# Kernel optimization log

Hardware: AMD Instinct MI355X
Metric: run time of the kernel (lower is better)

Reference implementation:

```python
import jax, jax.numpy as jnp
import numpy as np


def setup_inputs() -> dict:
    key = jax.random.key(0)
    k1, k2, k3 = jax.random.split(key, 3)
    B, D_IN, HIDDEN = 4096, 1024, 32768  # hidden = d_in * scale_size(32)
    x = jax.random.normal(k1, (B, D_IN), dtype=jnp.float32)
    W_enc = jax.random.normal(k2, (HIDDEN, D_IN), dtype=jnp.float32) * (1.0 / np.sqrt(D_IN))
    b_enc = jnp.zeros((HIDDEN,), dtype=jnp.float32)  # encoder.bias.data.zero_()
    # W_dec = encoder.weight.clone() then unit-norm rows (set_decoder_norm_to_unit_norm)
    W_dec = jax.random.normal(k3, (HIDDEN, D_IN), dtype=jnp.float32)
    W_dec = W_dec / (jnp.linalg.norm(W_dec, axis=1, keepdims=True) + jnp.finfo(jnp.float32).eps)
    b_dec = jnp.zeros((D_IN,), dtype=jnp.float32)
    return {"x": x, "W_enc": W_enc, "b_enc": b_enc, "W_dec": W_dec, "b_dec": b_dec, "k": 32}


def reference(x, W_enc, b_enc, W_dec, b_dec, k):
    # sae_in = x - b_dec; pre_acts = relu(encoder(sae_in))
    sae_in = x - b_dec
    pre_acts = jax.nn.relu(jnp.einsum('bd,hd->bh', sae_in, W_enc) + b_enc)  # [B, H]
    # topk_activation: keep top-k per row, zero elsewhere, then z @ W_dec.
    # Equivalent sparse decode: gather the k rows of W_dec and contract.
    topk_vals, topk_idx = jax.lax.top_k(pre_acts, k)  # [B, k]
    # x_reconstructed = z @ W_dec + b_dec  (z is the dense scatter of topk)
    x_rec = jnp.einsum('bk,bkd->bd', topk_vals, W_dec[topk_idx]) + b_dec
    return x_rec
```

## Files before the change

kernel.cpp:

```cpp
#include <hip/hip_runtime.h>
#include <hip/hip_bf16.h>
#include <stdint.h>
#include <stddef.h>


#define BROWS 4096
#define DIN   1024
#define HID   32768
#define KTOP  32
#define KC    48
#define PT    16

#define BM 256
#define BN 256
#define BK 64
#define NT (DIN / BK)

typedef short short8_t __attribute__((ext_vector_type(8)));
typedef float fx4 __attribute__((ext_vector_type(4)));

__device__ __forceinline__ unsigned short f2bf(float f) {
  unsigned u = __float_as_uint(f);
  u += 0x7FFFu + ((u >> 16) & 1u);
  return (unsigned short)(u >> 16);
}

__global__ __launch_bounds__(256) void conv_wc(const float* __restrict__ W,
                                               unsigned short* __restrict__ Wbc, int c0) {
  int base = (blockIdx.x * 256 + threadIdx.x) * 4;
  float4 v = *(const float4*)(W + (size_t)c0 * DIN + base);
  ushort4 o;
  o.x = f2bf(v.x); o.y = f2bf(v.y); o.z = f2bf(v.z); o.w = f2bf(v.w);
  *(ushort4*)(Wbc + base) = o;
}

__global__ __launch_bounds__(256) void prep_x(const float* __restrict__ x,
                                              const float* __restrict__ bdec,
                                              unsigned short* __restrict__ xbf) {
  int base = (blockIdx.x * 256 + threadIdx.x) * 4;
  int col = base & (DIN - 1);
  float4 xv = *(const float4*)(x + base);
  float4 bv = *(const float4*)(bdec + col);
  ushort4 o;
  o.x = f2bf(xv.x - bv.x); o.y = f2bf(xv.y - bv.y);
  o.z = f2bf(xv.z - bv.z); o.w = f2bf(xv.w - bv.w);
  *(ushort4*)(xbf + base) = o;
}

__global__ __launch_bounds__(256) void init_cand(unsigned* __restrict__ cand) {
  int i = blockIdx.x * 256 + threadIdx.x;
  if (i < BROWS * KC) cand[i] = 0u;
}


__device__ __forceinline__ void stage_half(const unsigned short* __restrict__ g0,
                                           unsigned short* l0, int t, int k0) {
  const int w6 = (t >> 6) << 6;
#pragma unroll
  for (int i = 0; i < 2; ++i) {
    const int l  = i * 512 + t;
    const int r  = l >> 3;
    const int cl = (l & 7) ^ (r & 7);
    const unsigned short* g = g0 + (size_t)r * DIN + k0 + cl * 8;
    unsigned short* ld = l0 + (size_t)(i * 512 + w6) * 8;
    __builtin_amdgcn_global_load_lds((const __attribute__((address_space(1))) unsigned int*)g,
                                     (__attribute__((address_space(3))) unsigned int*)ld,
                                     16, 0, 0);
  }
}

__device__ __forceinline__ void tile_step(int tt,
                                          const unsigned short* __restrict__ Ab,
                                          const unsigned short* __restrict__ Wb,
                                          unsigned short* bc, unsigned short* bn,
                                          fx4 (&acc)[8][4],
                                          int t, int l16, int quad, int wm, int wn) {
  const int k1 = (tt + 1) * BK;
  const int k2 = (tt + 2) * BK;
  if (tt < NT - 1) { asm volatile("s_waitcnt vmcnt(4)" ::: "memory"); }
  else             { asm volatile("s_waitcnt vmcnt(0)" ::: "memory"); }
  __builtin_amdgcn_s_barrier();
  const unsigned short* Ar = bc + wm * 8192;
  const unsigned short* Br = bc + 16384;
  short8_t a0[8], a1[8], bfv[4][2];
#pragma unroll
  for (int mt = 0; mt < 8; ++mt)
    a0[mt] = *(const short8_t*)(Ar + (mt * 16 + l16) * 64 + ((quad) ^ (l16 & 7)) * 8);
#pragma unroll
  for (int nt = 0; nt < 4; ++nt)
#pragma unroll
    for (int ks = 0; ks < 2; ++ks)
      bfv[nt][ks] = *(const short8_t*)(Br + (wn * 64 + nt * 16 + l16) * 64 +
                                       ((ks * 4 + quad) ^ (l16 & 7)) * 8);
  if (tt + 1 < NT) stage_half(Wb, bn + 16384, t, k1);
  __builtin_amdgcn_s_setprio(1);
#pragma unroll
  for (int mt = 0; mt < 8; ++mt) {
    acc[mt][0] = __builtin_amdgcn_mfma_f32_16x16x32_bf16(a0[mt], bfv[0][0], acc[mt][0], 0, 0, 0);
    acc[mt][1] = __builtin_amdgcn_mfma_f32_16x16x32_bf16(a0[mt], bfv[1][0], acc[mt][1], 0, 0, 0);
  }
  __builtin_amdgcn_s_setprio(0);
  __builtin_amdgcn_s_barrier();
  if (tt + 1 < NT) stage_half(Wb + 128 * DIN, bn + 24576, t, k1);
  __builtin_amdgcn_s_setprio(1);
#pragma unroll
  for (int mt = 0; mt < 8; ++mt) {
    acc[mt][2] = __builtin_amdgcn_mfma_f32_16x16x32_bf16(a0[mt], bfv[2][0], acc[mt][2], 0, 0, 0);
    acc[mt][3] = __builtin_amdgcn_mfma_f32_16x16x32_bf16(a0[mt], bfv[3][0], acc[mt][3], 0, 0, 0);
  }
  __builtin_amdgcn_s_setprio(0);
  __builtin_amdgcn_s_barrier();
#pragma unroll
  for (int mt = 0; mt < 8; ++mt)
    a1[mt] = *(const short8_t*)(Ar + (mt * 16 + l16) * 64 + ((4 + quad) ^ (l16 & 7)) * 8);
#pragma unroll
  for (int mt = 0; mt < 8; ++mt) { asm volatile("" : "+v"(a1[mt])); }
  __builtin_amdgcn_sched_barrier(0);
  __builtin_amdgcn_s_barrier();
  if (tt + 2 < NT) stage_half(Ab, bc, t, k2);
  __builtin_amdgcn_s_setprio(1);
#pragma unroll
  for (int mt = 0; mt < 8; ++mt) {
    acc[mt][0] = __builtin_amdgcn_mfma_f32_16x16x32_bf16(a1[mt], bfv[0][1], acc[mt][0], 0, 0, 0);
    acc[mt][1] = __builtin_amdgcn_mfma_f32_16x16x32_bf16(a1[mt], bfv[1][1], acc[mt][1], 0, 0, 0);
  }
  __builtin_amdgcn_s_setprio(0);
  __builtin_amdgcn_s_barrier();
  if (tt + 2 < NT) stage_half(Ab + 128 * DIN, bc + 8192, t, k2);
  __builtin_amdgcn_s_setprio(1);
#pragma unroll
  for (int mt = 0; mt < 8; ++mt) {
    acc[mt][2] = __builtin_amdgcn_mfma_f32_16x16x32_bf16(a1[mt], bfv[2][1], acc[mt][2], 0, 0, 0);
    acc[mt][3] = __builtin_amdgcn_mfma_f32_16x16x32_bf16(a1[mt], bfv[3][1], acc[mt][3], 0, 0, 0);
  }
  __builtin_amdgcn_s_setprio(0);
  __builtin_amdgcn_s_barrier();
}

__global__ __launch_bounds__(512, 2) void gemm_scores(
    const unsigned short* __restrict__ A,
    const unsigned short* __restrict__ W,
    const float* __restrict__ benc,
    unsigned short* __restrict__ scores,
    int Hc, int c0) {
  extern __shared__ unsigned short lds[];
  const int t    = threadIdx.x;
  const int lane = t & 63;
  const int wv   = t >> 6;
  const int wm   = wv >> 2;
  const int wn   = wv & 3;
  const int l16  = lane & 15;
  const int quad = lane >> 4;

  const int nwg  = (int)(gridDim.x * gridDim.y);
  const int orig = (int)(blockIdx.y * gridDim.x + blockIdx.x);
  const int q    = nwg >> 3, r8 = nwg & 7;
  const int xcd  = orig & 7, loc = orig >> 3;
  const int swz  = (xcd < r8 ? xcd * (q + 1) : r8 * (q + 1) + (xcd - r8) * q) + loc;
  const int bx   = swz % (int)gridDim.x;
  const int by   = swz / (int)gridDim.x;

  const int row0  = by * BM;
  const int colc0 = bx * BN;
  const unsigned short* Ab = A + (size_t)row0 * DIN;
  const unsigned short* Wb = W + (size_t)colc0 * DIN;

  unsigned short* buf0 = lds;
  unsigned short* buf1 = lds + 32768;

  fx4 acc[8][4];
  fx4 zero = {0.f, 0.f, 0.f, 0.f};
#pragma unroll
  for (int i = 0; i < 8; ++i)
#pragma unroll
    for (int j = 0; j < 4; ++j) acc[i][j] = zero;

  stage_half(Ab,            buf0,         t, 0);
  stage_half(Ab + 128*DIN,  buf0 + 8192,  t, 0);
  stage_half(Wb,            buf0 + 16384, t, 0);
  stage_half(Wb + 128*DIN,  buf0 + 24576, t, 0);
  stage_half(Ab,            buf1,         t, BK);
  stage_half(Ab + 128*DIN,  buf1 + 8192,  t, BK);

#pragma unroll 1
  for (int it = 0; it < NT / 2; ++it) {
    tile_step(2 * it,     Ab, Wb, buf0, buf1, acc, t, l16, quad, wm, wn);
    tile_step(2 * it + 1, Ab, Wb, buf1, buf0, acc, t, l16, quad, wm, wn);
  }

  const int colbase = colc0 + wn * 64;
  float bval[4];
#pragma unroll
  for (int nt = 0; nt < 4; ++nt) bval[nt] = benc[c0 + colbase + nt * 16 + l16];

  unsigned short* et = lds;
#pragma unroll
  for (int c = 0; c < 2; ++c) {
    __syncthreads();
    if (wm == c) {
#pragma unroll
      for (int mt = 0; mt < 8; ++mt)
#pragma unroll
        for (int nt = 0; nt < 4; ++nt) {
          const int col = wn * 64 + nt * 16 + l16;
          const int ch = col >> 3, cw = col & 7;
#pragma unroll
          for (int rg = 0; rg < 4; ++rg) {
            const int row = mt * 16 + quad * 4 + rg;
            float v = acc[mt][nt][rg] + bval[nt];
            et[row * 256 + ((ch ^ quad) * 8) + cw] = f2bf(v > 0.f ? v : 0.f);
          }
        }
    }
    __syncthreads();
    {
      const int row = t >> 2;
      const int cb  = (t & 3) * 8;
      const int xq  = (row >> 2) & 3;
      const size_t gro = (size_t)(row0 + c * 128 + row) * Hc + colc0;
#pragma unroll
      for (int i = 0; i < 8; ++i) {
        const int ch = cb + i;
        short8_t v = *(const short8_t*)(et + row * 256 + ((ch ^ xq) * 8));
        *(short8_t*)(scores + gro + ch * 8) = v;
      }
    }
  }
}

__global__ __launch_bounds__(128) void topk_cand(const unsigned short* __restrict__ scores,
                                                 int Hc, int c0,
                                                 unsigned* __restrict__ cand) {
  __shared__ unsigned lk[128 * 17];
  const int row = blockIdx.x;
  const int t = threadIdx.x;
  unsigned s[PT];
#pragma unroll
  for (int j = 0; j < PT; ++j) s[j] = 0u;

  const unsigned short* srow = scores + (size_t)row * Hc;
  for (int cb = t * 8; cb < Hc; cb += 128 * 8) {
    short8_t v = *(const short8_t*)(srow + cb);
    int gcb = c0 + cb;
#pragma unroll
    for (int e = 0; e < 8; ++e) {
      unsigned val = (unsigned)(unsigned short)v[e];
      unsigned key = (val << 16) | (unsigned)(0x7FFF - (gcb + e));
      if (key > s[PT - 1]) {
        unsigned prev = 0xFFFFFFFFu;
#pragma unroll
        for (int j = 0; j < PT; ++j) {
          unsigned sj = s[j];
          s[j] = (sj >= key) ? sj : (prev < key ? prev : key);
          prev = sj;
        }
      }
    }
  }
  if (t < KC) {
    unsigned key = cand[row * KC + t];
    if (key > s[PT - 1]) {
      unsigned prev = 0xFFFFFFFFu;
#pragma unroll
      for (int j = 0; j < PT; ++j) {
        unsigned sj = s[j];
        s[j] = (sj >= key) ? sj : (prev < key ? prev : key);
        prev = sj;
      }
    }
  }
#pragma unroll
  for (int j = 0; j < PT; ++j) lk[t * 17 + j] = s[j];
  __syncthreads();

  if (t < 64) {
    unsigned k0 = lk[t * 17];
    unsigned k1 = lk[(t + 64) * 17];
    int h0 = 0, h1 = 0;
    unsigned mywin = 0;
    for (int it = 0; it < KC; ++it) {
      unsigned wmax = (k0 > k1) ? k0 : k1;
#pragma unroll
      for (int off = 32; off >= 1; off >>= 1) {
        unsigned o = __shfl_down(wmax, (unsigned)off);
        if (o > wmax) wmax = o;
      }
      wmax = __shfl(wmax, 0);
      if (it == t) mywin = wmax;
      if (k0 == wmax)      { ++h0; k0 = (h0 < PT) ? lk[t * 17 + h0] : 0u; }
      else if (k1 == wmax) { ++h1; k1 = (h1 < PT) ? lk[(t + 64) * 17 + h1] : 0u; }
    }
    if (t < KC) cand[row * KC + t] = mywin;
  }
}

__global__ __launch_bounds__(256) void rescore_decode(
    const unsigned* __restrict__ cand,
    const float* __restrict__ x, const float* __restrict__ Wenc,
    const float* __restrict__ benc,
    const float* __restrict__ Wdec, const float* __restrict__ bdec,
    float* __restrict__ out) {
  __shared__ float xr[DIN];
  __shared__ double sc[KC];
  __shared__ int   scol[KC];
  __shared__ float fv[KTOP];
  __shared__ int   fi[KTOP];
  const int row = blockIdx.x, t = threadIdx.x;

  {
    float4 xv = *(const float4*)(x + (size_t)row * DIN + t * 4);
    float4 bv = *(const float4*)(bdec + t * 4);
    *(float4*)(xr + t * 4) = make_float4(xv.x - bv.x, xv.y - bv.y, xv.z - bv.z, xv.w - bv.w);
  }
  if (t < KC) scol[t] = 0x7FFF - (int)(cand[row * KC + t] & 0xFFFFu);
  if (t < KTOP) { fv[t] = 0.f; fi[t] = 0; }
  __syncthreads();

  const int wave = t >> 6, lane = t & 63;
  for (int j = wave; j < KC; j += 4) {
    int col = scol[j];
    const float* wr = Wenc + (size_t)col * DIN;
    double p = 0.0;
#pragma unroll
    for (int q = 0; q < 4; ++q) {
      int o = q * 256 + lane * 4;
      float4 w = *(const float4*)(wr + o);
      float4 xv = *(const float4*)(xr + o);
      p += (double)xv.x * (double)w.x + (double)xv.y * (double)w.y +
           (double)xv.z * (double)w.z + (double)xv.w * (double)w.w;
    }
#pragma unroll
    for (int off = 32; off >= 1; off >>= 1) p += __shfl_down(p, off);
    if (lane == 0) {
      double v = p + (double)benc[col];
      sc[j] = v > 0.0 ? v : 0.0;
    }
  }
  __syncthreads();

  if (t < KC) {
    double mv = sc[t];
    int mc = scol[t];
    int rank = 0;
    for (int j = 0; j < KC; ++j) {
      double oj = sc[j];
      if (oj > mv || (oj == mv && (scol[j] < mc || (scol[j] == mc && j < t)))) ++rank;
    }
    if (rank < KTOP) { fv[rank] = (float)mv; fi[rank] = mc; }
  }
  __syncthreads();

  const int c = t * 4;
  float4 bd = *(const float4*)(bdec + c);
  float a0 = bd.x, a1 = bd.y, a2 = bd.z, a3 = bd.w;
#pragma unroll 8
  for (int j = 0; j < KTOP; ++j) {
    float v = fv[j];
    float4 w = *(const float4*)(Wdec + (size_t)fi[j] * DIN + c);
    a0 += v * w.x; a1 += v * w.y; a2 += v * w.z; a3 += v * w.w;
  }
  *(float4*)(out + (size_t)row * DIN + c) = make_float4(a0, a1, a2, a3);
}

extern "C" void kernel_launch(void* const* d_in, const int* in_sizes, int n_in,
                              void* d_out, int out_size, void* d_ws, size_t ws_size,
                              hipStream_t stream) {
  const float* x    = (const float*)d_in[0];
  const float* Wenc = (const float*)d_in[1];
  const float* benc = (const float*)d_in[2];
  const float* Wdec = (const float*)d_in[3];
  const float* bdec = (const float*)d_in[4];
  float* out = (float*)d_out;

  char* ws = (char*)d_ws;
  unsigned short* xbf  = (unsigned short*)ws;
  unsigned*       cand = (unsigned*)(ws + (8u << 20));

  const size_t fixed = (size_t)(9u << 20);
  int Hc = HID;
  while (Hc > 256 &&
         fixed + (size_t)Hc * DIN * 2 + (size_t)BROWS * Hc * 2 > ws_size)
    Hc >>= 1;

  unsigned short* Wbc    = (unsigned short*)(ws + fixed);
  unsigned short* scores = (unsigned short*)(ws + fixed + (size_t)Hc * DIN * 2);

  static bool attr_set = false;
  if (!attr_set) {
    (void)hipFuncSetAttribute((const void*)gemm_scores,
                              hipFuncAttributeMaxDynamicSharedMemorySize, 131072);
    attr_set = true;
  }

  prep_x<<<BROWS * DIN / 1024, 256, 0, stream>>>(x, bdec, xbf);
  init_cand<<<(BROWS * KC + 255) / 256, 256, 0, stream>>>(cand);
  for (int c0 = 0; c0 < HID; c0 += Hc) {
    conv_wc<<<Hc, 256, 0, stream>>>(Wenc, Wbc, c0);
    gemm_scores<<<dim3(Hc / BN, BROWS / BM), 512, 131072, stream>>>(xbf, Wbc, benc, scores, Hc, c0);
    topk_cand<<<BROWS, 128, 0, stream>>>(scores, Hc, c0, cand);
  }
  rescore_decode<<<BROWS, 256, 0, stream>>>(cand, x, Wenc, benc, Wdec, bdec, out);
}
```

Measured before the change: 1.119 ms.

## Reload MFMA fragments per phase to cut register pressure, pad epilogue LDS

The GEMM inner step now keeps one set of A fragments and two B fragments at a time, reloading them from LDS before each half of the tile rather than holding a0/a1 plus all eight B fragments. Extra barriers are added so the prefetch of the next A tile can be moved to the final phase and issued as one batch. The epilogue staging buffer changes from an XOR swizzle to a padded row stride. The goal is to lower VGPR pressure and simplify addressing, at the cost of more LDS reads and more barriers per tile step.

Result: faster. 1.020 ms (-8.8%).

```diff
diff --git a/kernel.cpp b/kernel.cpp
--- a/kernel.cpp
+++ b/kernel.cpp
@@ -15,6 +15,7 @@
 #define BN 256
 #define BK 64
 #define NT (DIN / BK)
+#define EP 264
 
 typedef short short8_t __attribute__((ext_vector_type(8)));
 typedef float fx4 __attribute__((ext_vector_type(4)));
@@ -80,59 +81,73 @@
   if (tt < NT - 1) { asm volatile("s_waitcnt vmcnt(4)" ::: "memory"); }
   else             { asm volatile("s_waitcnt vmcnt(0)" ::: "memory"); }
   __builtin_amdgcn_s_barrier();
+
   const unsigned short* Ar = bc + wm * 8192;
-  const unsigned short* Br = bc + 16384;
-  short8_t a0[8], a1[8], bfv[4][2];
-#pragma unroll
-  for (int mt = 0; mt < 8; ++mt)
-    a0[mt] = *(const short8_t*)(Ar + (mt * 16 + l16) * 64 + ((quad) ^ (l16 & 7)) * 8);
-#pragma unroll
-  for (int nt = 0; nt < 4; ++nt)
-#pragma unroll
-    for (int ks = 0; ks < 2; ++ks)
-      bfv[nt][ks] = *(const short8_t*)(Br + (wn * 64 + nt * 16 + l16) * 64 +
-                                       ((ks * 4 + quad) ^ (l16 & 7)) * 8);
+  const unsigned short* Br = bc + 16384 + (wn * 64 + l16) * 64;
+  const int xs = l16 & 7;
+  short8_t a[8], b0, b1;
+
+#pragma unroll
+  for (int mt = 0; mt < 8; ++mt)
+    a[mt] = *(const short8_t*)(Ar + (mt * 16 + l16) * 64 + ((quad ^ xs) * 8));
+  b0 = *(const short8_t*)(Br + 0 * 1024 + ((quad ^ xs) * 8));
+  b1 = *(const short8_t*)(Br + 1 * 1024 + ((quad ^ xs) * 8));
   if (tt + 1 < NT) stage_half(Wb, bn + 16384, t, k1);
+  __builtin_amdgcn_s_barrier();
   __builtin_amdgcn_s_setprio(1);
 #pragma unroll
-  for (int mt = 0; mt < 8; ++mt) {
-    acc[mt][0] = __builtin_amdgcn_mfma_f32_16x16x32_bf16(a0[mt], bfv[0][0], acc[mt][0], 0, 0, 0);
-    acc[mt][1] = __builtin_amdgcn_mfma_f32_16x16x32_bf16(a0[mt], bfv[1][0], acc[mt][1], 0, 0, 0);
-  }
+  for (int mt = 0; mt < 8; ++mt)
+    acc[mt][0] = __builtin_amdgcn_mfma_f32_16x16x32_bf16(a[mt], b0, acc[mt][0], 0, 0, 0);
+#pragma unroll
+  for (int mt = 0; mt < 8; ++mt)
+    acc[mt][1] = __builtin_amdgcn_mfma_f32_16x16x32_bf16(a[mt], b1, acc[mt][1], 0, 0, 0);
   __builtin_amdgcn_s_setprio(0);
   __builtin_amdgcn_s_barrier();
+
+  b0 = *(const short8_t*)(Br + 2 * 1024 + ((quad ^ xs) * 8));
+  b1 = *(const short8_t*)(Br + 3 * 1024 + ((quad ^ xs) * 8));
   if (tt + 1 < NT) stage_half(Wb + 128 * DIN, bn + 24576, t, k1);
+  __builtin_amdgcn_s_barrier();
   __builtin_amdgcn_s_setprio(1);
 #pragma unroll
-  for (int mt = 0; mt < 8; ++mt) {
-    acc[mt][2] = __builtin_amdgcn_mfma_f32_16x16x32_bf16(a0[mt], bfv[2][0], acc[mt][2], 0, 0, 0);
-    acc[mt][3] = __builtin_amdgcn_mfma_f32_16x16x32_bf16(a0[mt], bfv[3][0], acc[mt][3], 0, 0, 0);
-  }
+  for (int mt = 0; mt < 8; ++mt)
+    acc[mt][2] = __builtin_amdgcn_mfma_f32_16x16x32_bf16(a[mt], b0, acc[mt][2], 0, 0, 0);
+#pragma unroll
+  for (int mt = 0; mt < 8; ++mt)
+    acc[mt][3] = __builtin_amdgcn_mfma_f32_16x16x32_bf16(a[mt], b1, acc[mt][3], 0, 0, 0);
   __builtin_amdgcn_s_setprio(0);
   __builtin_amdgcn_s_barrier();
-#pragma unroll
-  for (int mt = 0; mt < 8; ++mt)
-    a1[mt] = *(const short8_t*)(Ar + (mt * 16 + l16) * 64 + ((4 + quad) ^ (l16 & 7)) * 8);
-#pragma unroll
-  for (int mt = 0; mt < 8; ++mt) { asm volatile("" : "+v"(a1[mt])); }
-  __builtin_amdgcn_sched_barrier(0);
-  __builtin_amdgcn_s_barrier();
-  if (tt + 2 < NT) stage_half(Ab, bc, t, k2);
+
+#pragma unroll
+  for (int mt = 0; mt < 8; ++mt)
+    a[mt] = *(const short8_t*)(Ar + (mt * 16 + l16) * 64 + (((4 + quad) ^ xs) * 8));
+  b0 = *(const short8_t*)(Br + 0 * 1024 + (((4 + quad) ^ xs) * 8));
+  b1 = *(const short8_t*)(Br + 1 * 1024 + (((4 + quad) ^ xs) * 8));
+  __builtin_amdgcn_s_barrier();
   __builtin_amdgcn_s_setprio(1);
 #pragma unroll
-  for (int mt = 0; mt < 8; ++mt) {
-    acc[mt][0] = __builtin_amdgcn_mfma_f32_16x16x32_bf16(a1[mt], bfv[0][1], acc[mt][0], 0, 0, 0);
-    acc[mt][1] = __builtin_amdgcn_mfma_f32_16x16x32_bf16(a1[mt], bfv[1][1], acc[mt][1], 0, 0, 0);
-  }
+  for (int mt = 0; mt < 8; ++mt)
+    acc[mt][0] = __builtin_amdgcn_mfma_f32_16x16x32_bf16(a[mt], b0, acc[mt][0], 0, 0, 0);
+#pragma unroll
+  for (int mt = 0; mt < 8; ++mt)
+    acc[mt][1] = __builtin_amdgcn_mfma_f32_16x16x32_bf16(a[mt], b1, acc[mt][1], 0, 0, 0);
   __builtin_amdgcn_s_setprio(0);
   __builtin_amdgcn_s_barrier();
-  if (tt + 2 < NT) stage_half(Ab + 128 * DIN, bc + 8192, t, k2);
+
+  b0 = *(const short8_t*)(Br + 2 * 1024 + (((4 + quad) ^ xs) * 8));
+  b1 = *(const short8_t*)(Br + 3 * 1024 + (((4 + quad) ^ xs) * 8));
+  if (tt + 2 < NT) {
+    stage_half(Ab,             bc,        t, k2);
+    stage_half(Ab + 128 * DIN, bc + 8192, t, k2);
+  }
+  __builtin_amdgcn_s_barrier();
   __builtin_amdgcn_s_setprio(1);
 #pragma unroll
-  for (int mt = 0; mt < 8; ++mt) {
-    acc[mt][2] = __builtin_amdgcn_mfma_f32_16x16x32_bf16(a1[mt], bfv[2][1], acc[mt][2], 0, 0, 0);
-    acc[mt][3] = __builtin_amdgcn_mfma_f32_16x16x32_bf16(a1[mt], bfv[3][1], acc[mt][3], 0, 0, 0);
-  }
+  for (int mt = 0; mt < 8; ++mt)
+    acc[mt][2] = __builtin_amdgcn_mfma_f32_16x16x32_bf16(a[mt], b0, acc[mt][2], 0, 0, 0);
+#pragma unroll
+  for (int mt = 0; mt < 8; ++mt)
+    acc[mt][3] = __builtin_amdgcn_mfma_f32_16x16x32_bf16(a[mt], b1, acc[mt][3], 0, 0, 0);
   __builtin_amdgcn_s_setprio(0);
   __builtin_amdgcn_s_barrier();
 }
@@ -199,29 +214,26 @@
     __syncthreads();
     if (wm == c) {
 #pragma unroll
-      for (int mt = 0; mt < 8; ++mt)
-#pragma unroll
-        for (int nt = 0; nt < 4; ++nt) {
-          const int col = wn * 64 + nt * 16 + l16;
-          const int ch = col >> 3, cw = col & 7;
+      for (int nt = 0; nt < 4; ++nt) {
+        const int col = wn * 64 + nt * 16 + l16;
+#pragma unroll
+        for (int mt = 0; mt < 8; ++mt)
 #pragma unroll
           for (int rg = 0; rg < 4; ++rg) {
             const int row = mt * 16 + quad * 4 + rg;
             float v = acc[mt][nt][rg] + bval[nt];
-            et[row * 256 + ((ch ^ quad) * 8) + cw] = f2bf(v > 0.f ? v : 0.f);
+            et[row * EP + col] = f2bf(v > 0.f ? v : 0.f);
           }
-        }
+      }
     }
     __syncthreads();
     {
       const int row = t >> 2;
-      const int cb  = (t & 3) * 8;
-      const int xq  = (row >> 2) & 3;
       const size_t gro = (size_t)(row0 + c * 128 + row) * Hc + colc0;
 #pragma unroll
       for (int i = 0; i < 8; ++i) {
-        const int ch = cb + i;
-        short8_t v = *(const short8_t*)(et + row * 256 + ((ch ^ xq) * 8));
+        const int ch = (t & 3) * 8 + i;
+        short8_t v = *(const short8_t*)(et + row * EP + ch * 8);
         *(short8_t*)(scores + gro + ch * 8) = v;
       }
     }
```
